# Kernel tuning notes

Hardware: AMD Instinct MI355X
Metric: run time of the kernel (lower is better)

## Reference

```python
import jax, jax.numpy as jnp
import numpy as np

TEMP = 0.05
EPS = 1e-8  # torch.nn.CosineSimilarity default eps


def setup_inputs() -> dict:
    key = jax.random.key(0)
    k1, k2 = jax.random.split(key)
    N, D = 16384, 1024
    online_output = jax.random.normal(k1, (N, D), dtype=jnp.float32)
    target_output = jax.random.normal(k2, (N, D), dtype=jnp.float32)
    return {"online_output": online_output, "target_output": target_output}


def reference(online_output, target_output):
    # Original code builds the full [N, N] cosine-similarity matrix and takes
    # its diagonal; the diagonal equals the row-wise paired cosine similarity,
    # so we compute only the O(N*D) paired form (identical math).
    dot = jnp.sum(online_output * target_output, axis=-1)          # [N]
    n1 = jnp.linalg.norm(online_output, axis=-1)                    # [N]
    n2 = jnp.linalg.norm(target_output, axis=-1)                    # [N]
    cos = dot / (jnp.maximum(n1, EPS) * jnp.maximum(n2, EPS))       # [N]
    return (2.0 - 2.0 * cos).mean() / TEMP
```

## Files before the change

kernel.cpp:

```cpp
#include <hip/hip_runtime.h>

#define TEMP 0.05f
#define EPS 1e-8f
#define NROWS 16384
#define DDIM 1024
#define NBLOCKS (NROWS / 4)

__global__ __launch_bounds__(256) void byol_rows_kernel(
        const float* __restrict__ a, const float* __restrict__ b,
        float* __restrict__ partials) {
    const int wave = threadIdx.x >> 6;
    const int lane = threadIdx.x & 63;
    const int row  = blockIdx.x * 4 + wave;

    const float4* a4 = (const float4*)(a + (size_t)row * DDIM);
    const float4* b4 = (const float4*)(b + (size_t)row * DDIM);

    float dot = 0.f, aa = 0.f, bb = 0.f;
#pragma unroll
    for (int j = 0; j < 4; ++j) {
        float4 av = a4[lane + 64 * j];
        float4 bv = b4[lane + 64 * j];
        dot += av.x * bv.x + av.y * bv.y + av.z * bv.z + av.w * bv.w;
        aa  += av.x * av.x + av.y * av.y + av.z * av.z + av.w * av.w;
        bb  += bv.x * bv.x + bv.y * bv.y + bv.z * bv.z + bv.w * bv.w;
    }

#pragma unroll
    for (int off = 32; off > 0; off >>= 1) {
        dot += __shfl_down(dot, off, 64);
        aa  += __shfl_down(aa,  off, 64);
        bb  += __shfl_down(bb,  off, 64);
    }

    __shared__ float s[4];
    if (lane == 0) {
        float n1 = fmaxf(sqrtf(aa), EPS);
        float n2 = fmaxf(sqrtf(bb), EPS);
        float c  = dot / (n1 * n2);
        s[wave]  = 2.0f - 2.0f * c;
    }
    __syncthreads();
    if (threadIdx.x == 0) {
        partials[blockIdx.x] = s[0] + s[1] + s[2] + s[3];
    }
}

__global__ __launch_bounds__(256) void byol_final_kernel(
        const float* __restrict__ partials, float* __restrict__ out) {
    float sum = 0.f;
#pragma unroll
    for (int j = 0; j < NBLOCKS / 256; ++j)
        sum += partials[threadIdx.x + 256 * j];

#pragma unroll
    for (int off = 32; off > 0; off >>= 1)
        sum += __shfl_down(sum, off, 64);

    __shared__ float s[4];
    const int wave = threadIdx.x >> 6;
    const int lane = threadIdx.x & 63;
    if (lane == 0) s[wave] = sum;
    __syncthreads();
    if (threadIdx.x == 0) {
        out[0] = (s[0] + s[1] + s[2] + s[3]) * (1.0f / ((float)NROWS * TEMP));
    }
}

extern "C" void kernel_launch(void* const* d_in, const int* in_sizes, int n_in,
                              void* d_out, int out_size, void* d_ws, size_t ws_size,
                              hipStream_t stream) {
    const float* a = (const float*)d_in[0];
    const float* b = (const float*)d_in[1];
    float* out = (float*)d_out;
    float* partials = (float*)d_ws;

    byol_rows_kernel<<<NBLOCKS, 256, 0, stream>>>(a, b, partials);
    byol_final_kernel<<<1, 256, 0, stream>>>(partials, out);
}
```

Baseline: 141.5 us.

## Process four rows per wave with register double-buffered nontemporal loads

Each wave now handles four consecutive rows and prefetches the next row's data into registers while reducing the current one. Loads use nontemporal hints and the grid drops to 1024 blocks, which cuts per-block launch and reduction overhead. The cost is more registers per thread, fewer resident waves to hide memory latency, and redundant xor-shuffle reductions on every lane.

```diff
diff --git a/kernel.cpp b/kernel.cpp
--- a/kernel.cpp
+++ b/kernel.cpp
@@ -4,42 +4,71 @@
 #define EPS 1e-8f
 #define NROWS 16384
 #define DDIM 1024
-#define NBLOCKS (NROWS / 4)
+#define NBLOCKS 1024
+#define ROWS_PER_WAVE 4
+
+typedef float f32x4 __attribute__((ext_vector_type(4)));
 
 __global__ __launch_bounds__(256) void byol_rows_kernel(
         const float* __restrict__ a, const float* __restrict__ b,
         float* __restrict__ partials) {
     const int wave = threadIdx.x >> 6;
     const int lane = threadIdx.x & 63;
-    const int row  = blockIdx.x * 4 + wave;
+    const int gwave = blockIdx.x * 4 + wave;
+    const int row0  = gwave * ROWS_PER_WAVE;
 
-    const float4* a4 = (const float4*)(a + (size_t)row * DDIM);
-    const float4* b4 = (const float4*)(b + (size_t)row * DDIM);
+    const f32x4* a4 = (const f32x4*)(a) + (size_t)row0 * (DDIM / 4) + lane;
+    const f32x4* b4 = (const f32x4*)(b) + (size_t)row0 * (DDIM / 4) + lane;
+    const int rstride = DDIM / 4;
 
-    float dot = 0.f, aa = 0.f, bb = 0.f;
+    f32x4 an[4], bn[4];
 #pragma unroll
-    for (int j = 0; j < 4; ++j) {
-        float4 av = a4[lane + 64 * j];
-        float4 bv = b4[lane + 64 * j];
-        dot += av.x * bv.x + av.y * bv.y + av.z * bv.z + av.w * bv.w;
-        aa  += av.x * av.x + av.y * av.y + av.z * av.z + av.w * av.w;
-        bb  += bv.x * bv.x + bv.y * bv.y + bv.z * bv.z + bv.w * bv.w;
-    }
+    for (int j = 0; j < 4; ++j) an[j] = __builtin_nontemporal_load(&a4[64 * j]);
+#pragma unroll
+    for (int j = 0; j < 4; ++j) bn[j] = __builtin_nontemporal_load(&b4[64 * j]);
+
+    float loss = 0.f;
 
 #pragma unroll
-    for (int off = 32; off > 0; off >>= 1) {
-        dot += __shfl_down(dot, off, 64);
-        aa  += __shfl_down(aa,  off, 64);
-        bb  += __shfl_down(bb,  off, 64);
+    for (int r = 0; r < ROWS_PER_WAVE; ++r) {
+        f32x4 ac[4], bc[4];
+#pragma unroll
+        for (int j = 0; j < 4; ++j) { ac[j] = an[j]; bc[j] = bn[j]; }
+
+        if (r + 1 < ROWS_PER_WAVE) {
+            const f32x4* a4n = a4 + (size_t)(r + 1) * rstride;
+            const f32x4* b4n = b4 + (size_t)(r + 1) * rstride;
+#pragma unroll
+            for (int j = 0; j < 4; ++j) an[j] = __builtin_nontemporal_load(&a4n[64 * j]);
+#pragma unroll
+            for (int j = 0; j < 4; ++j) bn[j] = __builtin_nontemporal_load(&b4n[64 * j]);
+        }
+
+        float dot = 0.f, aa = 0.f, bb = 0.f;
+#pragma unroll
+        for (int j = 0; j < 4; ++j) {
+            dot += ac[j].x * bc[j].x + ac[j].y * bc[j].y
+                 + ac[j].z * bc[j].z + ac[j].w * bc[j].w;
+            aa  += ac[j].x * ac[j].x + ac[j].y * ac[j].y
+                 + ac[j].z * ac[j].z + ac[j].w * ac[j].w;
+            bb  += bc[j].x * bc[j].x + bc[j].y * bc[j].y
+                 + bc[j].z * bc[j].z + bc[j].w * bc[j].w;
+        }
+
+#pragma unroll
+        for (int off = 32; off > 0; off >>= 1) {
+            dot += __shfl_xor(dot, off, 64);
+            aa  += __shfl_xor(aa,  off, 64);
+            bb  += __shfl_xor(bb,  off, 64);
+        }
+
+        float n1 = fmaxf(sqrtf(aa), EPS);
+        float n2 = fmaxf(sqrtf(bb), EPS);
+        loss += 2.0f - 2.0f * (dot / (n1 * n2));
     }
 
     __shared__ float s[4];
-    if (lane == 0) {
-        float n1 = fmaxf(sqrtf(aa), EPS);
-        float n2 = fmaxf(sqrtf(bb), EPS);
-        float c  = dot / (n1 * n2);
-        s[wave]  = 2.0f - 2.0f * c;
-    }
+    if (lane == 0) s[wave] = loss;
     __syncthreads();
     if (threadIdx.x == 0) {
         partials[blockIdx.x] = s[0] + s[1] + s[2] + s[3];
```

Measured after the change: 141.6 us. About the same (+0.1%).

## Map one row per block with one float4 per thread and cross-wave reduction

Applied to the files above, without the earlier changes.

Each row is now processed by a full 256-thread block, where every thread loads a single float4 from each input, instead of one wave per row doing four loads per lane. The three partial sums are combined across waves through shared memory before the cosine is computed, and the finalize kernel sums 16384 per-row values. The aim is more blocks and more independent memory requests in flight for this bandwidth-bound reduction. In exchange, the grid is four times larger, each block pays a barrier, and each thread has less work to hide latency.

```diff
diff --git a/kernel.cpp b/kernel.cpp
--- a/kernel.cpp
+++ b/kernel.cpp
@@ -4,45 +4,48 @@
 #define EPS 1e-8f
 #define NROWS 16384
 #define DDIM 1024
-#define NBLOCKS (NROWS / 4)
 
-__global__ __launch_bounds__(256) void byol_rows_kernel(
+typedef float f32x4 __attribute__((ext_vector_type(4)));
+
+__global__ __launch_bounds__(256) void byol_row_kernel(
         const float* __restrict__ a, const float* __restrict__ b,
         float* __restrict__ partials) {
-    const int wave = threadIdx.x >> 6;
-    const int lane = threadIdx.x & 63;
-    const int row  = blockIdx.x * 4 + wave;
+    const int row  = blockIdx.x;
+    const int t    = threadIdx.x;
+    const int wave = t >> 6;
+    const int lane = t & 63;
 
-    const float4* a4 = (const float4*)(a + (size_t)row * DDIM);
-    const float4* b4 = (const float4*)(b + (size_t)row * DDIM);
+    const f32x4* a4 = (const f32x4*)(a) + (size_t)row * (DDIM / 4) + t;
+    const f32x4* b4 = (const f32x4*)(b) + (size_t)row * (DDIM / 4) + t;
 
-    float dot = 0.f, aa = 0.f, bb = 0.f;
-#pragma unroll
-    for (int j = 0; j < 4; ++j) {
-        float4 av = a4[lane + 64 * j];
-        float4 bv = b4[lane + 64 * j];
-        dot += av.x * bv.x + av.y * bv.y + av.z * bv.z + av.w * bv.w;
-        aa  += av.x * av.x + av.y * av.y + av.z * av.z + av.w * av.w;
-        bb  += bv.x * bv.x + bv.y * bv.y + bv.z * bv.z + bv.w * bv.w;
-    }
+    f32x4 av = *a4;
+    f32x4 bv = *b4;
+
+    float dot = av.x * bv.x + av.y * bv.y + av.z * bv.z + av.w * bv.w;
+    float aa  = av.x * av.x + av.y * av.y + av.z * av.z + av.w * av.w;
+    float bb  = bv.x * bv.x + bv.y * bv.y + bv.z * bv.z + bv.w * bv.w;
 
 #pragma unroll
     for (int off = 32; off > 0; off >>= 1) {
-        dot += __shfl_down(dot, off, 64);
-        aa  += __shfl_down(aa,  off, 64);
-        bb  += __shfl_down(bb,  off, 64);
+        dot += __shfl_xor(dot, off, 64);
+        aa  += __shfl_xor(aa,  off, 64);
+        bb  += __shfl_xor(bb,  off, 64);
     }
 
-    __shared__ float s[4];
+    __shared__ float s[12];
     if (lane == 0) {
-        float n1 = fmaxf(sqrtf(aa), EPS);
-        float n2 = fmaxf(sqrtf(bb), EPS);
-        float c  = dot / (n1 * n2);
-        s[wave]  = 2.0f - 2.0f * c;
+        s[wave]     = dot;
+        s[wave + 4] = aa;
+        s[wave + 8] = bb;
     }
     __syncthreads();
-    if (threadIdx.x == 0) {
-        partials[blockIdx.x] = s[0] + s[1] + s[2] + s[3];
+    if (t == 0) {
+        float d = s[0] + s[1] + s[2]  + s[3];
+        float x = s[4] + s[5] + s[6]  + s[7];
+        float y = s[8] + s[9] + s[10] + s[11];
+        float n1 = fmaxf(sqrtf(x), EPS);
+        float n2 = fmaxf(sqrtf(y), EPS);
+        partials[row] = 2.0f - 2.0f * (d / (n1 * n2));
     }
 }
 
@@ -50,7 +53,7 @@
         const float* __restrict__ partials, float* __restrict__ out) {
     float sum = 0.f;
 #pragma unroll
-    for (int j = 0; j < NBLOCKS / 256; ++j)
+    for (int j = 0; j < NROWS / 256; ++j)
         sum += partials[threadIdx.x + 256 * j];
 
 #pragma unroll
@@ -75,6 +78,6 @@
     float* out = (float*)d_out;
     float* partials = (float*)d_ws;
 
-    byol_rows_kernel<<<NBLOCKS, 256, 0, stream>>>(a, b, partials);
+    byol_row_kernel<<<NROWS, 256, 0, stream>>>(a, b, partials);
     byol_final_kernel<<<1, 256, 0, stream>>>(partials, out);
 }
```

Measured after the change: 142.3 us. No clear change (+0.6%).
